# Optimization experiments

Hardware: AMD Instinct MI355X
Metric: run time of the kernel (lower is better)

Reference implementation:

```python
import jax, jax.numpy as jnp
import numpy as np

B = 1048576       # batch
N_BLOCKS = 16     # n
M = 2             # m (positives counted in first M slots of each block)
BLOCK = 2         # 32 / n
Q = 2.0           # t, the 'q' scale applied to the max block


def _partial_activation(Y):
    """Vectorized equivalent of Net.partial_activation(Y, n=16, m=2, t=2).
    Y: [B, 32]. Returns (masked Y, succ scalar, train scalar)."""
    b, L = Y.shape
    Yb = Y.reshape(b, N_BLOCKS, BLOCK)
    # count of positive entries in the first M slots of each block -> [b, n]
    pos = jnp.sum((Yb[..., :M] > 0).astype(jnp.float32), axis=-1)
    minI = jnp.argmin(pos, axis=-1)   # first-occurrence, matches np.argmin
    maxI = jnp.argmax(pos, axis=-1)
    max_succ = jnp.take_along_axis(pos, maxI[:, None], axis=1)[:, 0] == M
    min_succ = jnp.take_along_axis(pos, minI[:, None], axis=1)[:, 0] == 0

    # mask: q on first M slots of the max block iff max_succ,
    #       0 on first M slots of the min block iff min_succ, else 1.
    blk = jnp.arange(N_BLOCKS)
    col = jnp.arange(BLOCK) < M                                   # [BLOCK]
    is_max = (blk[None, :] == maxI[:, None]) & max_succ[:, None]  # [b, n]
    is_min = (blk[None, :] == minI[:, None]) & min_succ[:, None]
    mask = jnp.where(is_max[..., None] & col, Q, 1.0)             # [b, n, BLOCK]
    mask = jnp.where(is_min[..., None] & col, 0.0, mask)
    mask = jax.lax.stop_gradient(mask.reshape(b, L))              # target.detach()
    out = Y * mask

    # train term: + positive entries of min block (when min not succ),
    #             - negative entries of max block (when max not succ).
    rows = jnp.arange(b)[:, None]
    k = jnp.arange(M)[None, :]
    ymin_c = Y[rows, minI[:, None] * M + k]       # condition uses *m index
    ymin_v = Y[rows, minI[:, None] * BLOCK + k]   # value uses *block index
    ymax_c = Y[rows, maxI[:, None] * M + k]
    ymax_v = Y[rows, maxI[:, None] * BLOCK + k]
    cmin = jnp.sum(ymin_v * (ymin_c > 0), axis=-1)
    cmax = -jnp.sum(ymax_v * (ymax_c < 0), axis=-1)
    train = jnp.sum(jnp.where(~min_succ, cmin, 0.0)
                    + jnp.where(~max_succ, cmax, 0.0))
    succ = jnp.mean((max_succ & min_succ).astype(jnp.float32))
    return out, succ, train


def setup_inputs() -> dict:
    key = jax.random.key(0)
    ks = jax.random.split(key, 7)
    x = jax.random.normal(ks[0], (B, 2), dtype=jnp.float32)
    def lin(kw, kb, out_f, in_f):
        bound = 1.0 / np.sqrt(in_f)
        W = jax.random.uniform(kw, (out_f, in_f), jnp.float32, -bound, bound)
        bias = jax.random.uniform(kb, (out_f,), jnp.float32, -bound, bound)
        return W, bias
    W1, b1 = lin(ks[1], ks[2], 32, 2)
    W2, b2 = lin(ks[3], ks[4], 32, 32)
    W3, b3 = lin(ks[5], ks[6], 2, 32)
    return {"x": x, "W1": W1, "b1": b1, "W2": W2, "b2": b2,
            "W3": W3, "b3": b3}


def reference(x, W1, b1, W2, b2, W3, b3):
    h1, s1, t1 = _partial_activation(x @ W1.T + b1)
    h2, s2, t2 = _partial_activation(h1 @ W2.T + b2)
    out = jax.nn.softmax(h2 @ W3.T + b3, axis=-1)
    return out, (s1 + s2) / 2.0, t1 + t2
```

## Files before the change

### kernel.cpp

```cpp
#include <hip/hip_runtime.h>

#define TPB 256

__device__ __forceinline__ void partial_act(float (&Y)[32], float& t_acc, int& s_cnt)
{
    int pos[16];
#pragma unroll
    for (int b = 0; b < 16; ++b)
        pos[b] = (Y[2 * b] > 0.0f ? 1 : 0) + (Y[2 * b + 1] > 0.0f ? 1 : 0);

    int minv = pos[0], maxv = pos[0];
    int minI = 0, maxI = 0;
    float ymin0 = Y[0], ymin1 = Y[1];
    float ymax0 = Y[0], ymax1 = Y[1];
#pragma unroll
    for (int b = 1; b < 16; ++b) {
        bool lt = pos[b] < minv;
        minv  = lt ? pos[b]       : minv;
        minI  = lt ? b            : minI;
        ymin0 = lt ? Y[2 * b]     : ymin0;
        ymin1 = lt ? Y[2 * b + 1] : ymin1;
        bool gt = pos[b] > maxv;
        maxv  = gt ? pos[b]       : maxv;
        maxI  = gt ? b            : maxI;
        ymax0 = gt ? Y[2 * b]     : ymax0;
        ymax1 = gt ? Y[2 * b + 1] : ymax1;
    }
    bool min_succ = (minv == 0);
    bool max_succ = (maxv == 2);

    float cmin = fmaxf(ymin0, 0.0f) + fmaxf(ymin1, 0.0f);
    float cmax = -(fminf(ymax0, 0.0f) + fminf(ymax1, 0.0f));
    t_acc += (min_succ ? 0.0f : cmin) + (max_succ ? 0.0f : cmax);
    s_cnt += (min_succ && max_succ) ? 1 : 0;

#pragma unroll
    for (int b = 0; b < 16; ++b) {
        bool ismax = max_succ && (b == maxI);
        bool ismin = min_succ && (b == minI);
        float mfac = ismax ? 2.0f : 1.0f;
        mfac = ismin ? 0.0f : mfac;
        Y[2 * b]     *= mfac;
        Y[2 * b + 1] *= mfac;
    }
}

__global__ __launch_bounds__(TPB, 3) void net_main(
    const float* __restrict__ x,
    const float* __restrict__ W1, const float* __restrict__ b1,
    const float* __restrict__ W2, const float* __restrict__ b2,
    const float* __restrict__ W3, const float* __restrict__ b3,
    float* __restrict__ out,
    float* __restrict__ t_part, int* __restrict__ c_part,
    unsigned* __restrict__ counter,
    int half, int nrows, double inv_denom)
{
    const int tid = threadIdx.x;
    const int r0  = blockIdx.x * TPB + tid;

    float t_acc = 0.0f;
    int   s_cnt = 0;

    if (r0 < half) {
        const int r1 = r0 + half;
        const float2 xa = reinterpret_cast<const float2*>(x)[r0];
        const float2 xb = reinterpret_cast<const float2*>(x)[r1];

        float A[32], B[32];
#pragma unroll
        for (int j = 0; j < 32; ++j) {
            const float w0 = W1[2 * j], w1 = W1[2 * j + 1], bb = b1[j];
            A[j] = fmaf(xa.y, w1, fmaf(xa.x, w0, bb));
            B[j] = fmaf(xb.y, w1, fmaf(xb.x, w0, bb));
        }

        partial_act(A, t_acc, s_cnt);
        partial_act(B, t_acc, s_cnt);

        float ZA[32], ZB[32];
#pragma unroll
        for (int j = 0; j < 32; ++j) {
            float a0 = b2[j];
            float a1 = b2[j];
#pragma unroll
            for (int k = 0; k < 32; ++k) {
                const float w = W2[32 * j + k];
                a0 = fmaf(A[k], w, a0);
                a1 = fmaf(B[k], w, a1);
            }
            ZA[j] = a0;
            ZB[j] = a1;
        }

        partial_act(ZA, t_acc, s_cnt);
        partial_act(ZB, t_acc, s_cnt);

        {
            float z0 = b3[0], z1 = b3[1];
            float y0 = b3[0], y1 = b3[1];
#pragma unroll
            for (int k = 0; k < 32; ++k) {
                const float wa = W3[k], wb = W3[32 + k];
                z0 = fmaf(ZA[k], wa, z0);
                z1 = fmaf(ZA[k], wb, z1);
                y0 = fmaf(ZB[k], wa, y0);
                y1 = fmaf(ZB[k], wb, y1);
            }
            float m0  = fmaxf(z0, z1);
            float e00 = __expf(z0 - m0);
            float e01 = __expf(z1 - m0);
            float i0  = 1.0f / (e00 + e01);
            float2 oa; oa.x = e00 * i0; oa.y = e01 * i0;
            reinterpret_cast<float2*>(out)[r0] = oa;

            float m1  = fmaxf(y0, y1);
            float e10 = __expf(y0 - m1);
            float e11 = __expf(y1 - m1);
            float i1  = 1.0f / (e10 + e11);
            float2 ob; ob.x = e10 * i1; ob.y = e11 * i1;
            reinterpret_cast<float2*>(out)[r1] = ob;
        }
    }

#pragma unroll
    for (int off = 32; off; off >>= 1) {
        t_acc += __shfl_down(t_acc, off);
        s_cnt += __shfl_down(s_cnt, off);
    }
    __shared__ float ts[TPB / 64];
    __shared__ int   cs[TPB / 64];
    __shared__ bool  amLast;
    const int wid  = tid >> 6;
    const int lane = tid & 63;
    if (lane == 0) { ts[wid] = t_acc; cs[wid] = s_cnt; }
    __syncthreads();
    if (tid == 0) {
        float tt = ts[0];
        int   cc = cs[0];
#pragma unroll
        for (int w = 1; w < TPB / 64; ++w) { tt += ts[w]; cc += cs[w]; }
        t_part[blockIdx.x] = tt;
        c_part[blockIdx.x] = cc;
        __threadfence();
        unsigned old = atomicAdd(counter, 1u);
        amLast = (old == gridDim.x - 1);
    }
    __syncthreads();

    if (amLast) {
        __threadfence();
        double t = 0.0;
        int    c = 0;
        const int nparts = gridDim.x;
        for (int i = tid; i < nparts; i += TPB) {
            t += (double)t_part[i];
            c += c_part[i];
        }
#pragma unroll
        for (int off = 32; off; off >>= 1) {
            t += __shfl_down(t, off);
            c += __shfl_down(c, off);
        }
        __shared__ double td[TPB / 64];
        __shared__ int    cd[TPB / 64];
        if (lane == 0) { td[wid] = t; cd[wid] = c; }
        __syncthreads();
        if (tid == 0) {
            double tt = 0.0;
            int    cc = 0;
#pragma unroll
            for (int w = 0; w < TPB / 64; ++w) { tt += td[w]; cc += cd[w]; }
            float* scal = out + (size_t)nrows * 2;
            scal[0] = (float)((double)cc * inv_denom);
            scal[1] = (float)tt;
        }
    }
}

extern "C" void kernel_launch(void* const* d_in, const int* in_sizes, int n_in,
                              void* d_out, int out_size, void* d_ws, size_t ws_size,
                              hipStream_t stream)
{
    const float* x  = (const float*)d_in[0];
    const float* W1 = (const float*)d_in[1];
    const float* b1 = (const float*)d_in[2];
    const float* W2 = (const float*)d_in[3];
    const float* b2 = (const float*)d_in[4];
    const float* W3 = (const float*)d_in[5];
    const float* b3 = (const float*)d_in[6];
    float* out = (float*)d_out;

    const int nrows   = in_sizes[0] / 2;
    const int half    = nrows / 2;
    const int nblocks = (half + TPB - 1) / TPB;

    float*    t_part  = (float*)d_ws;
    int*      c_part  = (int*)((char*)d_ws + (size_t)nblocks * sizeof(float));
    unsigned* counter = (unsigned*)((char*)d_ws + (size_t)nblocks * 2 * sizeof(float));

    hipMemsetAsync(counter, 0, sizeof(unsigned), stream);

    net_main<<<nblocks, TPB, 0, stream>>>(x, W1, b1, W2, b2, W3, b3,
                                          out, t_part, c_part, counter,
                                          half, nrows, 1.0 / (2.0 * (double)nrows));
}
```

Before: 147.5 us.

## Double-buffer W2 rows through scalar registers with inline s_load_dwordx16

After: 150.2 us. About the same (+1.8%).

```diff
diff --git a/kernel.cpp b/kernel.cpp
--- a/kernel.cpp
+++ b/kernel.cpp
@@ -1,6 +1,16 @@
 #include <hip/hip_runtime.h>
 
 #define TPB 256
+
+typedef float f32x16 __attribute__((ext_vector_type(16)));
+
+#define SLOAD16(dst, base, byteoff) \
+    asm volatile("s_load_dwordx16 %0, %1, %2" : "=s"(dst) : "s"(base), "i"(byteoff))
+
+#define SWAIT2(b0, b1) \
+    asm volatile("s_waitcnt lgkmcnt(0)" : "+s"(b0), "+s"(b1))
+#define SWAIT4(b0, b1, v0, v1) \
+    asm volatile("s_waitcnt lgkmcnt(0)" : "+s"(b0), "+s"(b1), "+v"(v0), "+v"(v1))
 
 __device__ __forceinline__ void partial_act(float (&Y)[32], float& t_acc, int& s_cnt)
 {
@@ -45,7 +55,7 @@
     }
 }
 
-__global__ __launch_bounds__(TPB, 3) void net_main(
+__global__ __launch_bounds__(TPB, 2) void net_main(
     const float* __restrict__ x,
     const float* __restrict__ W1, const float* __restrict__ b1,
     const float* __restrict__ W2, const float* __restrict__ b2,
@@ -66,30 +76,73 @@
         const float2 xa = reinterpret_cast<const float2*>(x)[r0];
         const float2 xb = reinterpret_cast<const float2*>(x)[r1];
 
-        float A[32], B[32];
+        f32x16 A0, A1, B0, B1;
+        SLOAD16(A0, W2, 0);
+        SLOAD16(A1, W2, 64);
+
+        int zi;
+        asm volatile("v_mov_b32 %0, 0" : "=v"(zi));
+
+        float YA[32], YB[32];
 #pragma unroll
         for (int j = 0; j < 32; ++j) {
             const float w0 = W1[2 * j], w1 = W1[2 * j + 1], bb = b1[j];
-            A[j] = fmaf(xa.y, w1, fmaf(xa.x, w0, bb));
-            B[j] = fmaf(xb.y, w1, fmaf(xb.x, w0, bb));
-        }
-
-        partial_act(A, t_acc, s_cnt);
-        partial_act(B, t_acc, s_cnt);
+            YA[j] = fmaf(xa.y, w1, fmaf(xa.x, w0, bb));
+            YB[j] = fmaf(xb.y, w1, fmaf(xb.x, w0, bb));
+        }
+
+        partial_act(YA, t_acc, s_cnt);
+        partial_act(YB, t_acc, s_cnt);
+
+        float b2r[32];
+#pragma unroll
+        for (int k = 0; k < 32; ++k)
+            b2r[k] = __int_as_float(__float_as_int(b2[k]) | zi);
 
         float ZA[32], ZB[32];
 #pragma unroll
-        for (int j = 0; j < 32; ++j) {
-            float a0 = b2[j];
-            float a1 = b2[j];
-#pragma unroll
-            for (int k = 0; k < 32; ++k) {
-                const float w = W2[32 * j + k];
-                a0 = fmaf(A[k], w, a0);
-                a1 = fmaf(B[k], w, a1);
-            }
-            ZA[j] = a0;
-            ZB[j] = a1;
+        for (int jj = 0; jj < 16; ++jj) {
+            const int j0 = 2 * jj, j1 = 2 * jj + 1;
+
+            SWAIT2(A0, A1);
+            SLOAD16(B0, W2, j1 * 128);
+            SLOAD16(B1, W2, j1 * 128 + 64);
+
+            float a0 = b2r[j0];
+            float a1 = b2r[j0];
+#pragma unroll
+            for (int k = 0; k < 16; ++k) {
+                a0 = fmaf(YA[k], A0[k], a0);
+                a1 = fmaf(YB[k], A0[k], a1);
+            }
+#pragma unroll
+            for (int k = 0; k < 16; ++k) {
+                a0 = fmaf(YA[16 + k], A1[k], a0);
+                a1 = fmaf(YB[16 + k], A1[k], a1);
+            }
+            ZA[j0] = a0;
+            ZB[j0] = a1;
+
+            SWAIT4(B0, B1, a0, a1);
+            if (jj < 15) {
+                SLOAD16(A0, W2, (j0 + 2) * 128);
+                SLOAD16(A1, W2, (j0 + 2) * 128 + 64);
+            }
+
+            float c0 = b2r[j1];
+            float c1 = b2r[j1];
+#pragma unroll
+            for (int k = 0; k < 16; ++k) {
+                c0 = fmaf(YA[k], B0[k], c0);
+                c1 = fmaf(YB[k], B0[k], c1);
+            }
+#pragma unroll
+            for (int k = 0; k < 16; ++k) {
+                c0 = fmaf(YA[16 + k], B1[k], c0);
+                c1 = fmaf(YB[16 + k], B1[k], c1);
+            }
+            ZA[j1] = c0;
+            ZB[j1] = c1;
         }
 
         partial_act(ZA, t_acc, s_cnt);
```
